# Performance work log

Hardware: AMD Instinct MI355X
Metric: run time of the kernel (lower is better)

## Reference

```python
import jax, jax.numpy as jnp
import numpy as np
from jax import lax

B, S, T = 16, 128, 128
E, H = 512, 1024
VIN, VOUT = 32000, 32000
NEG = jnp.float32(-1e10)


def lstm_cell(x, h, c, Wih, Whh, bih, bhh):
    # PyTorch gate order: i, f, g, o
    z = x @ Wih.T + h @ Whh.T + bih + bhh
    i, f, g, o = jnp.split(z, 4, axis=-1)
    c2 = jax.nn.sigmoid(f) * c + jax.nn.sigmoid(i) * jnp.tanh(g)
    h2 = jax.nn.sigmoid(o) * jnp.tanh(c2)
    return h2, c2


def setup_inputs() -> dict:
    key = jax.random.key(0)
    ks = jax.random.split(key, 20)
    s = 0.05
    nrm = lambda k, shp: (jax.random.normal(k, shp, dtype=jnp.float32) * s)
    return {
        "input_tokens": jax.random.randint(ks[0], (B, S), 0, VIN, dtype=jnp.int32),
        "output_tokens": jax.random.randint(ks[1], (B, T), 0, VOUT, dtype=jnp.int32),
        "mask": jax.random.randint(ks[2], (B, S), 0, 2, dtype=jnp.int32),
        "emb_in": nrm(ks[3], (VIN, E)),
        "emb_out": nrm(ks[4], (VOUT, E)),
        "enc_Wih": nrm(ks[5], (4 * H, E)),
        "enc_Whh": nrm(ks[6], (4 * H, H)),
        "enc_bih": nrm(ks[7], (4 * H,)),
        "enc_bhh": nrm(ks[8], (4 * H,)),
        "dec_Wih": nrm(ks[9], (4 * H, E + H)),
        "dec_Whh": nrm(ks[10], (4 * H, H)),
        "dec_bih": nrm(ks[11], (4 * H,)),
        "dec_bhh": nrm(ks[12], (4 * H,)),
        "attn_W": nrm(ks[13], (H, 2 * H)),
        "attn_b": nrm(ks[14], (H,)),
        "out_W": nrm(ks[15], (VOUT, H)),
        "out_b": nrm(ks[16], (VOUT,)),
    }


def reference(input_tokens, output_tokens, mask, emb_in, emb_out,
              enc_Wih, enc_Whh, enc_bih, enc_bhh,
              dec_Wih, dec_Whh, dec_bih, dec_bhh,
              attn_W, attn_b, out_W, out_b):
    # ---- encoder (single-layer LSTM, batch_first) ----
    xe = emb_in[input_tokens]  # [B,S,E]
    h0 = jnp.zeros((B, H), jnp.float32)

    def enc_step(carry, x):
        h, c = carry
        h, c = lstm_cell(x, h, c, enc_Wih, enc_Whh, enc_bih, enc_bhh)
        return (h, c), h

    (hT, cT), enc_states = lax.scan(enc_step, (h0, h0), xe.transpose(1, 0, 2))
    enc_out = enc_states.transpose(1, 0, 2)  # [B,S,H]

    # ---- attention mask fixup (as in Attention_Layer.forward) ----
    length = jnp.argmin(mask, axis=-1) - 1  # first 0 position minus 1
    mask2 = mask.at[jnp.arange(B), length].set(0)

    # ---- decoder scan over T-1 steps ----
    xd = emb_out[output_tokens[:, :-1]]  # [B,T-1,E]

    def dec_step(carry, x):
        h, c, a = carry
        xin = jnp.concatenate([x, a], axis=-1)  # [B, E+H]
        h2, c2 = lstm_cell(xin, h, c, dec_Wih, dec_Whh, dec_bih, dec_bhh)
        scores = jnp.einsum('bsh,bh->bs', enc_out, h2)
        scores = jnp.where(mask2 == 1, NEG, scores)
        probs = jax.nn.softmax(scores, axis=-1)
        ct = jnp.einsum('bs,bsh->bh', probs, enc_out)
        a2 = jnp.tanh(jnp.concatenate([ct, h2], axis=-1) @ attn_W.T + attn_b)
        logits = a2 @ out_W.T + out_b
        return (h2, c2, a2), logits

    a0 = jnp.zeros((B, H), jnp.float32)
    _, logits = lax.scan(dec_step, (hT, cT, a0), xd.transpose(1, 0, 2))
    return logits.transpose(1, 0, 2)  # [B, T-1, VOUT]
```

## Files before the change

### kernel.cpp

```cpp
#include <hip/hip_runtime.h>
#include <hip/hip_bf16.h>
#include <stdint.h>

typedef unsigned short u16;
typedef unsigned long long u64;
typedef __bf16 bf16x8v __attribute__((ext_vector_type(8)));
typedef float f32x4 __attribute__((ext_vector_type(4)));

#define B_ 16
#define S_ 128
#define T1_ 127
#define E_ 512
#define H_ 1024
#define H4_ 4096
#define V_ 32000
#define NEGBIG -1e10f
#define NBLK 512

__device__ __forceinline__ u16 f2bf(float f) {
    union { float f; unsigned u; } v; v.f = f;
    unsigned u = v.u;
    unsigned r = (u + 0x7fffu + ((u >> 16) & 1u)) >> 16;
    return (u16)r;
}
__device__ __forceinline__ float bf2f(u16 h) {
    union { unsigned u; float f; } v; v.u = ((unsigned)h) << 16;
    return v.f;
}
__device__ __forceinline__ float sigm(float x) { return 1.f / (1.f + expf(-x)); }
__device__ __forceinline__ float dot4(float4 a, float4 b) {
    return a.x * b.x + a.y * b.y + a.z * b.z + a.w * b.w;
}
__device__ __forceinline__ void pub2(float* p, float v0, float v1) {
    union { float f[2]; u64 u; } pk;
    pk.f[0] = v0; pk.f[1] = v1;
    atomicExch((u64*)p, pk.u);
}

__device__ __forceinline__ void gbar(int* bar, int ep, int bk) {
    asm volatile("s_waitcnt vmcnt(0) lgkmcnt(0)" ::: "memory");
    __syncthreads();
    if (threadIdx.x == 0) {
        const int g1 = bk & 63, g2 = g1 >> 3;
        int old = atomicAdd(&bar[g1 * 16], 1);
        if (old == ep * 8 - 1) {
            int old2 = atomicAdd(&bar[1024 + g2 * 16], 1);
            if (old2 == ep * 8 - 1) {
                int old3 = atomicAdd(&bar[1152], 1);
                if (old3 == ep * 8 - 1) {
#pragma unroll
                    for (int j = 0; j < 8; ++j) atomicExch(&bar[1216 + j * 16], ep);
                }
            }
        }
        while (__hip_atomic_load(&bar[1216 + (bk & 7) * 16], __ATOMIC_RELAXED,
                                 __HIP_MEMORY_SCOPE_SYSTEM) < ep)
            __builtin_amdgcn_s_sleep(2);
    }
    __syncthreads();
}


__global__ __launch_bounds__(256) void f32_to_bf16_k(const float* __restrict__ src,
                                                     u16* __restrict__ dst, int n4) {
    int idx = blockIdx.x * 256 + threadIdx.x;
    if (idx >= n4) return;
    float4 v = ((const float4*)src)[idx];
    unsigned lo = (unsigned)f2bf(v.x) | ((unsigned)f2bf(v.y) << 16);
    unsigned hi = (unsigned)f2bf(v.z) | ((unsigned)f2bf(v.w) << 16);
    uint2 pk; pk.x = lo; pk.y = hi;
    *(uint2*)(dst + (size_t)idx * 4) = pk;
}

__global__ __launch_bounds__(128) void split3_rows_k(const float* __restrict__ src,
                                                     int srcStride,
                                                     u16* __restrict__ dst, int nrows,
                                                     int offH2, int offLo) {
    int j = blockIdx.x;
    if (j >= nrows) return;
    int tid = threadIdx.x;
    float4 v = *(const float4*)(src + (size_t)j * srcStride + tid * 4);
    u16 h0 = f2bf(v.x), h1 = f2bf(v.y), h2 = f2bf(v.z), h3 = f2bf(v.w);
    u16 l0 = f2bf(v.x - bf2f(h0)), l1 = f2bf(v.y - bf2f(h1));
    u16 l2 = f2bf(v.z - bf2f(h2)), l3 = f2bf(v.w - bf2f(h3));
    uint2 ph; ph.x = (unsigned)h0 | ((unsigned)h1 << 16); ph.y = (unsigned)h2 | ((unsigned)h3 << 16);
    uint2 pl; pl.x = (unsigned)l0 | ((unsigned)l1 << 16); pl.y = (unsigned)l2 | ((unsigned)l3 << 16);
    u16* base = dst + (size_t)j * 1536 + tid * 4;
    *(uint2*)(base) = ph;
    *(uint2*)(base + offH2) = ph;
    *(uint2*)(base + offLo) = pl;
}

__global__ __launch_bounds__(256) void split3_1024_k(const float* __restrict__ src,
                                                     int srcStride,
                                                     u16* __restrict__ dst,
                                                     int offH2, int offLo) {
    int j = blockIdx.x, tid = threadIdx.x;
    float4 v = *(const float4*)(src + (size_t)j * srcStride + tid * 4);
    u16 h0 = f2bf(v.x), h1 = f2bf(v.y), h2 = f2bf(v.z), h3 = f2bf(v.w);
    u16 l0 = f2bf(v.x - bf2f(h0)), l1 = f2bf(v.y - bf2f(h1));
    u16 l2 = f2bf(v.z - bf2f(h2)), l3 = f2bf(v.w - bf2f(h3));
    uint2 ph; ph.x = (unsigned)h0 | ((unsigned)h1 << 16); ph.y = (unsigned)h2 | ((unsigned)h3 << 16);
    uint2 pl; pl.x = (unsigned)l0 | ((unsigned)l1 << 16); pl.y = (unsigned)l2 | ((unsigned)l3 << 16);
    u16* base = dst + (size_t)j * 3072 + tid * 4;
    *(uint2*)(base) = ph;
    *(uint2*)(base + offH2) = ph;
    *(uint2*)(base + offLo) = pl;
}

__global__ __launch_bounds__(128) void gather_split_k(const int* __restrict__ toks,
                                                      const float* __restrict__ emb,
                                                      u16* __restrict__ A, int nrows) {
    int m = blockIdx.x;
    if (m >= nrows) return;
    int tIdx = m >> 4, b = m & 15;
    int tok = toks[b * 128 + tIdx];
    int tid = threadIdx.x;
    float4 v = *(const float4*)(emb + (size_t)tok * E_ + tid * 4);
    u16 h0 = f2bf(v.x), h1 = f2bf(v.y), h2 = f2bf(v.z), h3 = f2bf(v.w);
    u16 l0 = f2bf(v.x - bf2f(h0)), l1 = f2bf(v.y - bf2f(h1));
    u16 l2 = f2bf(v.z - bf2f(h2)), l3 = f2bf(v.w - bf2f(h3));
    uint2 ph; ph.x = (unsigned)h0 | ((unsigned)h1 << 16); ph.y = (unsigned)h2 | ((unsigned)h3 << 16);
    uint2 pl; pl.x = (unsigned)l0 | ((unsigned)l1 << 16); pl.y = (unsigned)l2 | ((unsigned)l3 << 16);
    u16* base = A + (size_t)m * 1536 + tid * 4;
    *(uint2*)(base) = ph;
    *(uint2*)(base + 512) = ph;
    *(uint2*)(base + 1024) = pl;
}

__global__ __launch_bounds__(256) void init_k(float* __restrict__ zero1,
                                              int* __restrict__ zero2,
                                              const int* __restrict__ mask,
                                              int* __restrict__ mask2) {
    int idx = blockIdx.x * 256 + threadIdx.x;
    float4 z = {0.f, 0.f, 0.f, 0.f};
    if (idx < 12288) ((float4*)zero1)[idx] = z;
    if (idx < 2048) { int4 zi = {0, 0, 0, 0}; ((int4*)zero2)[idx] = zi; }
    if (blockIdx.x == 0 && threadIdx.x < 16) {
        int b = threadIdx.x;
        int first0 = 128;
        for (int s = 0; s < 128; ++s) {
            if (mask[b * 128 + s] == 0) { first0 = s; break; }
        }
        if (first0 == 128) first0 = 0;
        int len = first0 - 1;
        int ix = (len < 0) ? 127 : len;
        for (int s = 0; s < 128; ++s) mask2[b * 128 + s] = mask[b * 128 + s];
        mask2[b * 128 + ix] = 0;
    }
}


#define GLD_LDS(g, l) \
    __builtin_amdgcn_global_load_lds((const __attribute__((address_space(1))) void*)(g), \
                                     (__attribute__((address_space(3))) void*)(l), 16, 0, 0)

template <int MODE>
__global__ __launch_bounds__(256) void gemm_bt(const u16* __restrict__ A,
                                               const u16* __restrict__ Bt,
                                               float* __restrict__ C,
                                               const float* __restrict__ bias1,
                                               const float* __restrict__ bias2,
                                               int M, int N, int K) {
    __shared__ u16 As[128 * 32];
    __shared__ u16 Bs[128 * 32];
    const int tid = threadIdx.x;
    const int bm = blockIdx.x, bn = blockIdx.y;
    const int lane = tid & 63, w = tid >> 6;
    const int wm = (w >> 1) * 64, wn = (w & 1) * 64;
    f32x4 acc[4][4] = {};

    const int r0 = tid >> 2;
    const int c0 = (tid & 3) * 8;
    const u16* ga0 = A + (size_t)(bm * 128 + r0) * K + c0;
    const u16* ga1 = A + (size_t)(bm * 128 + 64 + r0) * K + c0;
    const u16* gb0 = Bt + (size_t)(bn * 128 + r0) * K + c0;
    const u16* gb1 = Bt + (size_t)(bn * 128 + 64 + r0) * K + c0;
    u16* lA0 = As + tid * 8;
    u16* lA1 = As + 2048 + tid * 8;
    u16* lB0 = Bs + tid * 8;
    u16* lB1 = Bs + 2048 + tid * 8;

    const int fl = lane & 15, kg = lane >> 4;

    for (int k0 = 0; k0 < K; k0 += 32) {
        __syncthreads();
        GLD_LDS(ga0 + k0, lA0);
        GLD_LDS(ga1 + k0, lA1);
        GLD_LDS(gb0 + k0, lB0);
        GLD_LDS(gb1 + k0, lB1);
        __syncthreads();
        bf16x8v af[4], bfv[4];
#pragma unroll
        for (int i = 0; i < 4; ++i)
            af[i] = *(const bf16x8v*)(As + (wm + i * 16 + fl) * 32 + kg * 8);
#pragma unroll
        for (int j = 0; j < 4; ++j)
            bfv[j] = *(const bf16x8v*)(Bs + (wn + j * 16 + fl) * 32 + kg * 8);
#pragma unroll
        for (int i = 0; i < 4; ++i)
#pragma unroll
            for (int j = 0; j < 4; ++j)
                acc[i][j] = __builtin_amdgcn_mfma_f32_16x16x32_bf16(af[i], bfv[j], acc[i][j], 0, 0, 0);
    }

    const int coll = lane & 15;
    const int rowb = (lane >> 4) * 4;
#pragma unroll
    for (int i = 0; i < 4; ++i) {
#pragma unroll
        for (int j = 0; j < 4; ++j) {
#pragma unroll
            for (int r = 0; r < 4; ++r) {
                int m = bm * 128 + wm + i * 16 + rowb + r;
                int n = bn * 128 + wn + j * 16 + coll;
                float v = acc[i][j][r];
                if (MODE == 1) {
                    int tt = m >> 4, bb = m & 15;
                    if (tt < T1_) C[((size_t)bb * T1_ + tt) * V_ + n] = v + bias1[n];
                } else if (MODE == 2) {
                    if (m < M) {
                        int tt = m >> 4, bb = m & 15;
                        int g = n >> 10, d = n & 1023;
                        C[(((size_t)tt * 512 + (d >> 1)) * 16 + bb) * 8 + g * 2 +
                          (d & 1)] = v + bias1[n] + bias2[n];
                    }
                } else {
                    int b = m >> 7, s = m & 127;
                    C[(((size_t)(n >> 1) * 16 + b) * 128 + s) * 2 + (n & 1)] = v;
                }
            }
        }
    }
}


__global__ __launch_bounds__(256, 2) void enc_persist(
    const float* __restrict__ pre, const float* __restrict__ Whh,
    const float* __restrict__ h0zero, float* __restrict__ c,
    float* __restrict__ enc_out, int* bar) {
    __shared__ float4 red4[4 * 64 * 17];
    __shared__ float zred[256];
    const int bk = blockIdx.x;
    const int tid = threadIdx.x;
    const int wv = tid >> 6, lane = tid & 63;
    const int k0 = wv * 256 + lane * 4;

    float4 wr[2][4];
#pragma unroll
    for (int dd = 0; dd < 2; ++dd) {
        int d = (bk << 1) + dd;
#pragma unroll
        for (int g = 0; g < 4; ++g)
            wr[dd][g] = *(const float4*)(Whh + (size_t)(g * 1024 + d) * H_ + k0);
    }

    int ep = 0;
    for (int t = 0; t < 128; ++t) {
        const float* xsrc;
        size_t xstr;
        if (t == 0) { xsrc = h0zero; xstr = H_; }
        else { xsrc = enc_out + (size_t)(t - 1) * H_; xstr = (size_t)128 * H_; }

        float prz[8];
        if (tid < 16) {
            const float* pb = pre + ((size_t)t * 512 + bk) * 128 + tid * 8;
#pragma unroll
            for (int q = 0; q < 8; ++q) prz[q] = pb[q];
        }

        float hloc0 = 0.f, hloc1 = 0.f;
        for (int dd = 0; dd < 2; ++dd) {
            float4 part[16];
#pragma unroll
            for (int b = 0; b < 16; ++b) {
                float4 hv = *(const float4*)(xsrc + (size_t)b * xstr + k0);
                part[b].x = dot4(wr[dd][0], hv);
                part[b].y = dot4(wr[dd][1], hv);
                part[b].z = dot4(wr[dd][2], hv);
                part[b].w = dot4(wr[dd][3], hv);
            }
#pragma unroll
            for (int b = 0; b < 16; ++b) red4[(wv * 64 + lane) * 17 + b] = part[b];
            __syncthreads();
            {
                int v = tid & 63, wq = tid >> 6;
                const float* rf = (const float*)red4;
                float s = 0.f;
#pragma unroll 8
                for (int l = 0; l < 64; ++l) s += rf[(wq * 64 + l) * 68 + v];
                zred[wq * 64 + v] = s;
            }
            __syncthreads();
            if (tid < 16) {
                int b = tid;
                const int d = (bk << 1) + dd;
                float zz[4];
#pragma unroll
                for (int g = 0; g < 4; ++g) {
                    float s = zred[b * 4 + g] + zred[64 + b * 4 + g] +
                              zred[128 + b * 4 + g] + zred[192 + b * 4 + g];
                    zz[g] = s + prz[g * 2 + dd];
                }
                float co = c[b * H_ + d];
                float c2 = sigm(zz[1]) * co + sigm(zz[0]) * tanhf(zz[2]);
                float h2 = sigm(zz[3]) * tanhf(c2);
                c[b * H_ + d] = c2;
                if (dd == 0) hloc0 = h2; else hloc1 = h2;
            }
            __syncthreads();
        }
        if (tid < 16)
            pub2(&enc_out[((size_t)tid * 128 + t) * H_ + (bk << 1)], hloc0, hloc1);
        ++ep;
        gbar(bar, ep, bk);
    }
}


__global__ __launch_bounds__(256, 2) void dec_persist(
    const float* __restrict__ pre, const float* __restrict__ Whh,
    const float* __restrict__ WihFull, const float* __restrict__ attn_W,
    const float* __restrict__ attn_b, const float* __restrict__ enc_out,
    const float* __restrict__ PE2,
    float* __restrict__ h_ring, float* __restrict__ a_ring,
    float* __restrict__ scores_ring, const float* __restrict__ a0zero,
    float* __restrict__ c, const int* __restrict__ mask2,
    u16* __restrict__ a2bf, int* bar) {
    __shared__ float4 red4[4 * 64 * 17];
    __shared__ float zred[256];
    __shared__ float ps2[2048];
    const int bk = blockIdx.x;
    const int tid = threadIdx.x;
    const int wv = tid >> 6, lane = tid & 63;
    const int kq = (wv & 1) * 512 + lane * 8;
    const bool isA = wv >= 2;

    float4 wr[2][4][2];
#pragma unroll
    for (int dd = 0; dd < 2; ++dd) {
        int d = (bk << 1) + dd;
#pragma unroll
        for (int g = 0; g < 4; ++g) {
            int j = g * 1024 + d;
            const float* wsrc = isA ? (WihFull + (size_t)j * 1536 + 512 + kq)
                                    : (Whh + (size_t)j * H_ + kq);
            wr[dd][g][0] = *(const float4*)(wsrc);
            wr[dd][g][1] = *(const float4*)(wsrc + 4);
        }
    }
    const int ksl = wv * 256 + lane * 4;
    float4 wa2h[2];
#pragma unroll
    for (int dd = 0; dd < 2; ++dd)
        wa2h[dd] = *(const float4*)(attn_W + (size_t)((bk << 1) + dd) * 2048 + 1024 + ksl);

    int ep = 0;
    for (int t = 0; t < T1_; ++t) {
        const float* hsrc;
        size_t hstr;
        if (t == 0) { hsrc = enc_out + (size_t)127 * H_; hstr = (size_t)128 * H_; }
        else { hsrc = h_ring + (size_t)(t - 1) * B_ * H_; hstr = H_; }
        const float* asrc = (t == 0) ? a0zero : (a_ring + (size_t)(t - 1) * B_ * H_);
        float* hcur = h_ring + (size_t)t * B_ * H_;
        float* acur = a_ring + (size_t)t * B_ * H_;
        float* srow = scores_ring + (size_t)t * 2048;

        float prz[8];
        if (tid < 16) {
            const float* pb = pre + ((size_t)t * 512 + bk) * 128 + tid * 8;
#pragma unroll
            for (int q = 0; q < 8; ++q) prz[q] = pb[q];
        }

        const float* xsrc1 = isA ? asrc : hsrc;
        const size_t xstr1 = isA ? (size_t)H_ : hstr;
        float hloc0 = 0.f, hloc1 = 0.f;
        for (int dd = 0; dd < 2; ++dd) {
            float4 part[16];
#pragma unroll
            for (int b = 0; b < 16; ++b) {
                float4 x0 = *(const float4*)(xsrc1 + (size_t)b * xstr1 + kq);
                float4 x1 = *(const float4*)(xsrc1 + (size_t)b * xstr1 + kq + 4);
                part[b].x = dot4(wr[dd][0][0], x0) + dot4(wr[dd][0][1], x1);
                part[b].y = dot4(wr[dd][1][0], x0) + dot4(wr[dd][1][1], x1);
                part[b].z = dot4(wr[dd][2][0], x0) + dot4(wr[dd][2][1], x1);
                part[b].w = dot4(wr[dd][3][0], x0) + dot4(wr[dd][3][1], x1);
            }
#pragma unroll
            for (int b = 0; b < 16; ++b) red4[(wv * 64 + lane) * 17 + b] = part[b];
            __syncthreads();
            {
                int v = tid & 63, wq = tid >> 6;
                const float* rf = (const float*)red4;
                float s = 0.f;
#pragma unroll 8
                for (int l = 0; l < 64; ++l) s += rf[(wq * 64 + l) * 68 + v];
                zred[wq * 64 + v] = s;
            }
            __syncthreads();
            if (tid < 16) {
                int b = tid;
                const int d = (bk << 1) + dd;
                float zz[4];
#pragma unroll
                for (int g = 0; g < 4; ++g) {
                    float s = zred[b * 4 + g] + zred[64 + b * 4 + g] +
                              zred[128 + b * 4 + g] + zred[192 + b * 4 + g];
                    zz[g] = s + prz[g * 2 + dd];
                }
                float co = c[b * H_ + d];
                float c2 = sigm(zz[1]) * co + sigm(zz[0]) * tanhf(zz[2]);
                float h2 = sigm(zz[3]) * tanhf(c2);
                c[b * H_ + d] = c2;
                if (dd == 0) hloc0 = h2; else hloc1 = h2;
            }
            __syncthreads();
        }
        if (tid < 16) pub2(&hcur[tid * H_ + (bk << 1)], hloc0, hloc1);
        ++ep;
        gbar(bar, ep, bk);

        {
            const int sb = bk & 15;
            const int s = ((bk >> 4) << 2) + wv;
            const float* er = enc_out + ((size_t)sb * 128 + s) * H_;
            const float* hr = hcur + (size_t)sb * H_;
            const int kk = lane * 16;
            float sc = 0.f;
#pragma unroll
            for (int q = 0; q < 4; ++q) {
                float4 e = *(const float4*)(er + kk + q * 4);
                float4 h = *(const float4*)(hr + kk + q * 4);
                sc += dot4(e, h);
            }
#pragma unroll
            for (int off = 32; off; off >>= 1) sc += __shfl_xor(sc, off);
            if (lane == 0) {
                float val = (mask2[sb * 128 + s] == 1) ? NEGBIG : sc;
                atomicExch((unsigned*)&srow[sb * 128 + s], __float_as_uint(val));
            }
        }
        ++ep;
        gbar(bar, ep, bk);

        {
            float4 s0 = *(const float4*)(srow + tid * 8);
            float4 s1 = *(const float4*)(srow + tid * 8 + 4);
            *(float4*)(ps2 + tid * 8) = s0;
            *(float4*)(ps2 + tid * 8 + 4) = s1;
        }
        __syncthreads();
        {
            const int b = tid >> 4, l16 = tid & 15;
            float* pr = ps2 + b * 128 + l16 * 8;
            float m8 = pr[0];
#pragma unroll
            for (int q = 1; q < 8; ++q) m8 = fmaxf(m8, pr[q]);
#pragma unroll
            for (int off = 8; off; off >>= 1) m8 = fmaxf(m8, __shfl_xor(m8, off, 16));
            float e[8], ssum = 0.f;
#pragma unroll
            for (int q = 0; q < 8; ++q) { e[q] = expf(pr[q] - m8); ssum += e[q]; }
#pragma unroll
            for (int off = 8; off; off >>= 1) ssum += __shfl_xor(ssum, off, 16);
            float inv = 1.f / ssum;
            const float* pe = PE2 + (((size_t)bk * 16 + b) * 128 + l16 * 8) * 2;
            float pe0 = 0.f, pe1 = 0.f;
#pragma unroll
            for (int q = 0; q < 8; ++q) {
                float pq = e[q] * inv;
                pe0 += pq * pe[q * 2];
                pe1 += pq * pe[q * 2 + 1];
            }
#pragma unroll
            for (int off = 8; off; off >>= 1) {
                pe0 += __shfl_xor(pe0, off, 16);
                pe1 += __shfl_xor(pe1, off, 16);
            }
            if (l16 == 0) { zred[64 + b * 2] = pe0; zred[64 + b * 2 + 1] = pe1; }
        }
        float aloc0 = 0.f, aloc1 = 0.f;
        for (int dd = 0; dd < 2; ++dd) {
            float partA[16];
#pragma unroll
            for (int b = 0; b < 16; ++b) {
                float4 hv = *(const float4*)(hcur + (size_t)b * H_ + ksl);
                partA[b] = dot4(wa2h[dd], hv);
            }
#pragma unroll
            for (int q = 0; q < 4; ++q)
                red4[(wv * 64 + lane) * 17 + q] =
                    make_float4(partA[q * 4], partA[q * 4 + 1], partA[q * 4 + 2], partA[q * 4 + 3]);
            __syncthreads();
            if (tid < 64) {
                int v = tid & 15, wq = tid >> 4;
                const float* rf = (const float*)red4;
                float s = 0.f;
#pragma unroll 8
                for (int l = 0; l < 64; ++l) s += rf[(wq * 64 + l) * 68 + v];
                zred[wq * 16 + v] = s;
            }
            __syncthreads();
            if (tid < 16) {
                int b = tid;
                float v = zred[b] + zred[16 + b] + zred[32 + b] + zred[48 + b] +
                          zred[64 + b * 2 + dd] + attn_b[(bk << 1) + dd];
                v = tanhf(v);
                if (dd == 0) aloc0 = v; else aloc1 = v;
            }
            __syncthreads();
        }
        if (tid < 16) {
            pub2(&acur[tid * H_ + (bk << 1)], aloc0, aloc1);
            unsigned pk2 = (unsigned)f2bf(aloc0) | ((unsigned)f2bf(aloc1) << 16);
            *(unsigned*)&a2bf[((size_t)(t * 16 + tid)) * H_ + (bk << 1)] = pk2;
        }
        ++ep;
        gbar(bar, ep, bk);
    }
}


extern "C" void kernel_launch(void* const* d_in, const int* in_sizes, int n_in,
                              void* d_out, int out_size, void* d_ws, size_t ws_size,
                              hipStream_t stream) {
    const int* in_tok = (const int*)d_in[0];
    const int* out_tok = (const int*)d_in[1];
    const int* mask = (const int*)d_in[2];
    const float* emb_in = (const float*)d_in[3];
    const float* emb_out = (const float*)d_in[4];
    const float* enc_Wih = (const float*)d_in[5];
    const float* enc_Whh = (const float*)d_in[6];
    const float* enc_bih = (const float*)d_in[7];
    const float* enc_bhh = (const float*)d_in[8];
    const float* dec_Wih = (const float*)d_in[9];
    const float* dec_Whh = (const float*)d_in[10];
    const float* dec_bih = (const float*)d_in[11];
    const float* dec_bhh = (const float*)d_in[12];
    const float* attn_W = (const float*)d_in[13];
    const float* attn_b = (const float*)d_in[14];
    const float* out_W = (const float*)d_in[15];
    const float* out_b = (const float*)d_in[16];
    float* out = (float*)d_out;

    char* p = (char*)d_ws;
    auto alloc = [&](size_t bytes) {
        char* r = p;
        p += (bytes + 255) & ~(size_t)255;
        return r;
    };
    u16* A_enc3 = (u16*)alloc((size_t)2048 * 1536 * 2);
    u16* A_dec3 = (u16*)alloc((size_t)2048 * 1536 * 2);
    u16* W_e3 = (u16*)alloc((size_t)4096 * 1536 * 2);
    u16* W_d3 = (u16*)alloc((size_t)4096 * 1536 * 2);
    u16* Wo = (u16*)alloc((size_t)32000 * 1024 * 2);
    float* enc_pre = (float*)alloc((size_t)2048 * 4096 * 4);
    float* dec_pre = (float*)alloc((size_t)2048 * 4096 * 4);
    float* enc_out = (float*)alloc((size_t)16 * 128 * 1024 * 4);
    u16* a2bf = (u16*)alloc((size_t)2048 * 1024 * 2);
    u16* A3pe = (u16*)alloc((size_t)2048 * 3072 * 2);
    u16* Wpe3 = (u16*)alloc((size_t)1024 * 3072 * 2);
    float* PE2 = (float*)alloc((size_t)1024 * 16 * 128 * 4);
    float* h0 = (float*)alloc(16 * 1024 * 4);
    float* c = (float*)alloc(16 * 1024 * 4);
    float* a0 = (float*)alloc(16 * 1024 * 4);
    int* barE = (int*)alloc(4096 * 4);
    int* barD = (int*)alloc(4096 * 4);
    int* mask2 = (int*)alloc(16 * 128 * 4);

    float* h_ring = (float*)A_enc3;
    float* a_ring = h_ring + (size_t)128 * B_ * H_;
    float* scores_ring = a_ring + (size_t)128 * B_ * H_;

    init_k<<<48, 256, 0, stream>>>(h0, barE, mask, mask2);

    split3_rows_k<<<4096, 128, 0, stream>>>(enc_Wih, 512, W_e3, 4096, 1024, 512);
    split3_rows_k<<<4096, 128, 0, stream>>>(dec_Wih, 1536, W_d3, 4096, 1024, 512);
    split3_1024_k<<<1024, 256, 0, stream>>>(attn_W, 2048, Wpe3, 2048, 1024);
    f32_to_bf16_k<<<32000, 256, 0, stream>>>(out_W, Wo, 32000 * 1024 / 4);
    gather_split_k<<<2048, 128, 0, stream>>>(in_tok, emb_in, A_enc3, 2048);
    gather_split_k<<<2032, 128, 0, stream>>>(out_tok, emb_out, A_dec3, 2032);

    gemm_bt<2><<<dim3(16, 32), 256, 0, stream>>>(A_enc3, W_e3, enc_pre, enc_bih, enc_bhh,
                                                 2048, 4096, 1536);
    gemm_bt<2><<<dim3(16, 32), 256, 0, stream>>>(A_dec3, W_d3, dec_pre, dec_bih, dec_bhh,
                                                 2048, 4096, 1536);

    enc_persist<<<512, 256, 0, stream>>>(enc_pre, enc_Whh, h0, c, enc_out, barE);

    split3_1024_k<<<2048, 256, 0, stream>>>(enc_out, 1024, A3pe, 1024, 2048);
    gemm_bt<3><<<dim3(16, 8), 256, 0, stream>>>(A3pe, Wpe3, PE2, nullptr, nullptr,
                                                2048, 1024, 3072);

    dec_persist<<<512, 256, 0, stream>>>(dec_pre, dec_Whh, dec_Wih, attn_W, attn_b,
                                         enc_out, PE2, h_ring, a_ring, scores_ring,
                                         a0, c, mask2, a2bf, barD);

    gemm_bt<1><<<dim3(16, 250), 256, 0, stream>>>(a2bf, Wo, out, out_b, nullptr,
                                                  2048, 32000, 1024);
}
```

Before: 4.640 ms.

## Split grid barrier into arrive/wait and overlap independent loads with barrier wait

Splits the software grid barrier into separate arrive and wait phases so work that does not depend on other blocks can run while waiting. The encoder prefetches the next step's precomputed gate inputs between arrive and wait. The decoder loads its encoder-output rows and computes the attention-projection partial dot products on h during the barrier waits. The aim is to hide latency on the serial per-timestep critical path, at the cost of more live registers.

```diff
diff --git a/kernel.cpp b/kernel.cpp
--- a/kernel.cpp
+++ b/kernel.cpp
@@ -37,7 +37,7 @@
     atomicExch((u64*)p, pk.u);
 }
 
-__device__ __forceinline__ void gbar(int* bar, int ep, int bk) {
+__device__ __forceinline__ void gbar_arrive(int* bar, int ep, int bk) {
     asm volatile("s_waitcnt vmcnt(0) lgkmcnt(0)" ::: "memory");
     __syncthreads();
     if (threadIdx.x == 0) {
@@ -53,6 +53,10 @@
                 }
             }
         }
+    }
+}
+__device__ __forceinline__ void gbar_wait(int* bar, int ep, int bk) {
+    if (threadIdx.x == 0) {
         while (__hip_atomic_load(&bar[1216 + (bk & 7) * 16], __ATOMIC_RELAXED,
                                  __HIP_MEMORY_SCOPE_SYSTEM) < ep)
             __builtin_amdgcn_s_sleep(2);
@@ -255,19 +259,19 @@
             wr[dd][g] = *(const float4*)(Whh + (size_t)(g * 1024 + d) * H_ + k0);
     }
 
+    float prz[8];
+    if (tid < 16) {
+        const float* pb = pre + ((size_t)0 * 512 + bk) * 128 + tid * 8;
+#pragma unroll
+        for (int q = 0; q < 8; ++q) prz[q] = pb[q];
+    }
+
     int ep = 0;
     for (int t = 0; t < 128; ++t) {
         const float* xsrc;
         size_t xstr;
         if (t == 0) { xsrc = h0zero; xstr = H_; }
         else { xsrc = enc_out + (size_t)(t - 1) * H_; xstr = (size_t)128 * H_; }
-
-        float prz[8];
-        if (tid < 16) {
-            const float* pb = pre + ((size_t)t * 512 + bk) * 128 + tid * 8;
-#pragma unroll
-            for (int q = 0; q < 8; ++q) prz[q] = pb[q];
-        }
 
         float hloc0 = 0.f, hloc1 = 0.f;
         for (int dd = 0; dd < 2; ++dd) {
@@ -313,7 +317,18 @@
         if (tid < 16)
             pub2(&enc_out[((size_t)tid * 128 + t) * H_ + (bk << 1)], hloc0, hloc1);
         ++ep;
-        gbar(bar, ep, bk);
+        gbar_arrive(bar, ep, bk);
+        float przn[8];
+        if (tid < 16 && t + 1 < 128) {
+            const float* pb = pre + ((size_t)(t + 1) * 512 + bk) * 128 + tid * 8;
+#pragma unroll
+            for (int q = 0; q < 8; ++q) przn[q] = pb[q];
+        }
+        gbar_wait(bar, ep, bk);
+        if (tid < 16 && t + 1 < 128) {
+#pragma unroll
+            for (int q = 0; q < 8; ++q) prz[q] = przn[q];
+        }
     }
 }
 
@@ -355,6 +370,9 @@
     for (int dd = 0; dd < 2; ++dd)
         wa2h[dd] = *(const float4*)(attn_W + (size_t)((bk << 1) + dd) * 2048 + 1024 + ksl);
 
+    const int sb = bk & 15;
+    const int ss = ((bk >> 4) << 2) + wv;
+
     int ep = 0;
     for (int t = 0; t < T1_; ++t) {
         const float* hsrc;
@@ -419,30 +437,36 @@
         }
         if (tid < 16) pub2(&hcur[tid * H_ + (bk << 1)], hloc0, hloc1);
         ++ep;
-        gbar(bar, ep, bk);
-
+        gbar_arrive(bar, ep, bk);
+        float4 er4[4];
         {
-            const int sb = bk & 15;
-            const int s = ((bk >> 4) << 2) + wv;
-            const float* er = enc_out + ((size_t)sb * 128 + s) * H_;
-            const float* hr = hcur + (size_t)sb * H_;
-            const int kk = lane * 16;
+            const float* er = enc_out + ((size_t)sb * 128 + ss) * H_ + lane * 16;
+#pragma unroll
+            for (int q = 0; q < 4; ++q) er4[q] = *(const float4*)(er + q * 4);
+        }
+        gbar_wait(bar, ep, bk);
+
+        {
+            const float* hr = hcur + (size_t)sb * H_ + lane * 16;
             float sc = 0.f;
 #pragma unroll
-            for (int q = 0; q < 4; ++q) {
-                float4 e = *(const float4*)(er + kk + q * 4);
-                float4 h = *(const float4*)(hr + kk + q * 4);
-                sc += dot4(e, h);
-            }
+            for (int q = 0; q < 4; ++q) sc += dot4(er4[q], *(const float4*)(hr + q * 4));
 #pragma unroll
             for (int off = 32; off; off >>= 1) sc += __shfl_xor(sc, off);
             if (lane == 0) {
-                float val = (mask2[sb * 128 + s] == 1) ? NEGBIG : sc;
-                atomicExch((unsigned*)&srow[sb * 128 + s], __float_as_uint(val));
+                float val = (mask2[sb * 128 + ss] == 1) ? NEGBIG : sc;
+                atomicExch((unsigned*)&srow[sb * 128 + ss], __float_as_uint(val));
             }
         }
         ++ep;
-        gbar(bar, ep, bk);
+        gbar_arrive(bar, ep, bk);
+        float partA[2][16];
+#pragma unroll
+        for (int dd = 0; dd < 2; ++dd)
+#pragma unroll
+            for (int b = 0; b < 16; ++b)
+                partA[dd][b] = dot4(wa2h[dd], *(const float4*)(hcur + (size_t)b * H_ + ksl));
+        gbar_wait(bar, ep, bk);
 
         {
             float4 s0 = *(const float4*)(srow + tid * 8);
@@ -482,16 +506,11 @@
         }
         float aloc0 = 0.f, aloc1 = 0.f;
         for (int dd = 0; dd < 2; ++dd) {
-            float partA[16];
-#pragma unroll
-            for (int b = 0; b < 16; ++b) {
-                float4 hv = *(const float4*)(hcur + (size_t)b * H_ + ksl);
-                partA[b] = dot4(wa2h[dd], hv);
-            }
 #pragma unroll
             for (int q = 0; q < 4; ++q)
                 red4[(wv * 64 + lane) * 17 + q] =
-                    make_float4(partA[q * 4], partA[q * 4 + 1], partA[q * 4 + 2], partA[q * 4 + 3]);
+                    make_float4(partA[dd][q * 4], partA[dd][q * 4 + 1],
+                                partA[dd][q * 4 + 2], partA[dd][q * 4 + 3]);
             __syncthreads();
             if (tid < 64) {
                 int v = tid & 15, wq = tid >> 4;
@@ -517,7 +536,8 @@
             *(unsigned*)&a2bf[((size_t)(t * 16 + tid)) * H_ + (bk << 1)] = pk2;
         }
         ++ep;
-        gbar(bar, ep, bk);
+        gbar_arrive(bar, ep, bk);
+        gbar_wait(bar, ep, bk);
     }
 }
 
```

New measurement: 4.448 ms. 1.04x faster.
